# Kernel optimization log

Measured on AMD Instinct MI355X. Metric: run time of the kernel, lower is better.

Reference implementation:

```python
import jax, jax.numpy as jnp
import numpy as np

B, T, U, K, CDIM, S, M = 128, 600, 96, 10, 80, 512, 20
D1 = 3 + CDIM        # rnn1 input: x_t (3) + attention window w (CDIM)
D2 = 3 + S + CDIM    # rnn2 / rnn3 input: x_t + prev rnn out + w
OUT_DIM = 1 + 6 * M


def setup_inputs() -> dict:
    key = jax.random.key(0)
    ks = jax.random.split(key, 16)
    g = lambda k, shape: jax.random.normal(k, shape, jnp.float32) * 0.05
    z = lambda n: jnp.zeros((n,), jnp.float32)
    return {
        "x": jax.random.normal(ks[0], (B, T, 3), jnp.float32),
        "c_vec": jax.random.uniform(ks[1], (B, U, CDIM), jnp.float32),
        # FF cell 1 (input dim D1)
        "W_jx1": g(ks[2], (D1, S)), "b_jx1": z(S),
        "W_jh1": g(ks[3], (S, S)),  "b_jh1": z(S),
        "W_kx1": g(ks[4], (D1, S)), "b_kx1": z(S),
        "W_kh1": g(ks[5], (S, S)),  "b_kh1": z(S),
        # FF cell 2 (input dim D2) -- also used for the 3rd RNN (source reuses self.rnn2)
        "W_jx2": g(ks[6], (D2, S)), "b_jx2": z(S),
        "W_jh2": g(ks[7], (S, S)),  "b_jh2": z(S),
        "W_kx2": g(ks[8], (D2, S)), "b_kx2": z(S),
        "W_kh2": g(ks[9], (S, S)),  "b_kh2": z(S),
        # attention window head: S -> 3K
        "W_win": g(ks[10], (S, 3 * K)), "b_win": z(3 * K),
        # output head: S -> 1 + 6M
        "W_lin": g(ks[11], (S, OUT_DIM)), "b_lin": z(OUT_DIM),
    }


def _ff(inp, h, Wjx, bjx, Wjh, bjh, Wkx, bkx, Wkh, bkh):
    # custom gated cell: out = j*(1-h) + (1-k)*h
    j = jax.nn.sigmoid(inp @ Wjx + bjx + h @ Wjh + bjh)
    k = jax.nn.sigmoid(inp @ Wkx + bkx + h @ Wkh + bkh)
    return j * (1.0 - h) + (1.0 - k) * h


def reference(x, c_vec,
              W_jx1, b_jx1, W_jh1, b_jh1, W_kx1, b_kx1, W_kh1, b_kh1,
              W_jx2, b_jx2, W_jh2, b_jh2, W_kx2, b_kx2, W_kh2, b_kh2,
              W_win, b_win, W_lin, b_lin):
    u = jnp.arange(U, dtype=x.dtype)  # [U]

    def step(carry, xt):
        h1, h2, h3, kappa, w = carry  # h*: [B,S], kappa: [B,K], w: [B,CDIM]
        in1 = jnp.concatenate([xt, w], axis=-1)
        h1 = _ff(in1, h1, W_jx1, b_jx1, W_jh1, b_jh1, W_kx1, b_kx1, W_kh1, b_kh1)
        kg = h1 @ W_win + b_win                       # [B, 3K]
        a_hat, be_hat, k_hat = jnp.split(kg, 3, axis=1)
        alpha = jnp.exp(a_hat)                        # [B,K]
        beta = jnp.exp(be_hat)
        kappa = kappa + jnp.exp(k_hat)
        # phi[b,u] = sum_k alpha * exp(-beta * (kappa - u)^2)
        phi = jnp.sum(alpha[:, :, None] *
                      jnp.exp(-beta[:, :, None] * (kappa[:, :, None] - u) ** 2),
                      axis=1)                          # [B,U]
        w = jnp.einsum('bu,buc->bc', phi, c_vec)      # [B,CDIM]
        in2 = jnp.concatenate([xt, h1, w], axis=-1)
        h2 = _ff(in2, h2, W_jx2, b_jx2, W_jh2, b_jh2, W_kx2, b_kx2, W_kh2, b_kh2)
        in3 = jnp.concatenate([xt, h2, w], axis=-1)
        # source bug kept faithfully: third RNN reuses rnn2's weights
        h3 = _ff(in3, h3, W_jx2, b_jx2, W_jh2, b_jh2, W_kx2, b_kx2, W_kh2, b_kh2)
        return (h1, h2, h3, kappa, w), h3

    zS = jnp.zeros((B, S), x.dtype)
    init = (zS, zS, zS, jnp.zeros((B, K), x.dtype), jnp.zeros((B, CDIM), x.dtype))
    _, ys = jax.lax.scan(step, init, jnp.swapaxes(x, 0, 1))  # ys: [T,B,S]
    out_cat = jnp.swapaxes(ys, 0, 1).reshape(B * T, S)
    return out_cat @ W_lin + b_lin                    # [B*T, 1+6M]
```

## Files before the change

### kernel.cpp

```cpp
#include <hip/hip_runtime.h>
#include <hip/hip_bf16.h>

typedef __bf16 bf16;
typedef __bf16 bf16x8 __attribute__((ext_vector_type(8)));
typedef float  f32x4  __attribute__((ext_vector_type(4)));

#define AS1 __attribute__((address_space(1)))
#define AS3 __attribute__((address_space(3)))

#define NT   600
#define NB   128
#define NS   512
#define NU   96
#define NK   10
#define NC   80
#define NOUT 121

#define W1X_J 0
#define W1W_J 16384
#define W1H_J 65536
#define W1X_K 327680
#define W1W_K 344064
#define W1H_K 393216
#define W2X_J 655360
#define W2W_J 671744
#define W2A_J 720896
#define W2H_J 983040
#define W2X_K 1245184
#define W2W_K 1261568
#define W2A_K 1310720
#define W2H_K 1572864
#define WWIN  1835008
#define WLIN  1851392

#define BIAS_BYTE_OFF 3833856
#define H_BYTE_OFF    3842048
#define HBUF 65536
#define FLAG_BYTE_OFF 4659200
#define BAR_BYTE_OFF  4659264

#define HSTRIDE 520

#define AUX_SC0   1
#define AUX_SC0S1 17

__device__ __forceinline__ float ldIn(const void* q, long i, int isF32) {
  if (isF32) return ((const float*)q)[i];
  return (float)((const bf16*)q)[i];
}

struct KParams {
  const void* x;
  const void* c_vec;
  const void* b_win;
  const void* b_lin;
  const bf16* W;
  const float* bias;
  bf16* h1; bf16* h2; bf16* h3;
  void* out;
  const int* flag;
  int* bar;
};

template <int AUX>
__device__ __forceinline__ void stage_tile_async(const bf16* g, bf16* lds, int tid) {
  const int w = tid >> 6, lane = tid & 63;
#pragma unroll
  for (int r = 0; r < 4; ++r) {
    const int row = (w << 2) + r;
    __builtin_amdgcn_global_load_lds(
        (const AS1 void*)(g + (size_t)row * NS + (size_t)lane * 8),
        (AS3 void*)(lds + (size_t)row * HSTRIDE), 16, 0, AUX);
  }
}

__device__ __forceinline__ void group_arrive(int* gb) {
  __syncthreads();
  if (threadIdx.x == 0) {
    if ((__hip_atomic_fetch_add(gb, 1, __ATOMIC_RELAXED, __HIP_MEMORY_SCOPE_AGENT) & 31) == 31)
      __hip_atomic_fetch_add(gb + 8, 1, __ATOMIC_RELAXED, __HIP_MEMORY_SCOPE_AGENT);
  }
}
__device__ __forceinline__ void group_wait(int* gb, int target) {
  if (threadIdx.x == 0) {
    while (__hip_atomic_load(gb + 8, __ATOMIC_RELAXED, __HIP_MEMORY_SCOPE_AGENT) < target)
      __builtin_amdgcn_s_sleep(1);
  }
  __syncthreads();
  __atomic_signal_fence(__ATOMIC_ACQ_REL);
}

__device__ __forceinline__ void storeH(unsigned* dst, unsigned v, bool fast) {
  if (fast) *dst = v;
  else __hip_atomic_store(dst, v, __ATOMIC_RELAXED, __HIP_MEMORY_SCOPE_AGENT);
}

__global__ void sniff_kernel(const unsigned short* w, int* flag) {
  __shared__ int cnt;
  if (threadIdx.x == 0) cnt = 0;
  __syncthreads();
  int c = 0;
  for (int i = threadIdx.x; i < 8192; i += 256) {
    unsigned e = (w[2 * i] >> 7) & 0xFF;
    if (e == 0xFF || e < 96) c++;
  }
  atomicAdd(&cnt, c);
  __syncthreads();
  if (threadIdx.x == 0) *flag = (cnt > 512) ? 1 : 0;
}

__global__ void prep_kernel(const void* Wjx1, const void* Wjh1, const void* Wkx1, const void* Wkh1,
                            const void* Wjx2, const void* Wjh2, const void* Wkx2, const void* Wkh2,
                            const void* Wwin, const void* Wlin,
                            const void* bjx1, const void* bjh1, const void* bkx1, const void* bkh1,
                            const void* bjx2, const void* bjh2, const void* bkx2, const void* bkh2,
                            bf16* W, float* bias,
                            bf16* h1, bf16* h2, bf16* h3, int* bar,
                            const int* flag) {
  const int isF32 = *flag;
  const int r = blockIdx.y;
  const int e = blockIdx.x * 256 + threadIdx.x;
  if (r == 16) {
    if (e < 512) {
      bias[e]        = ldIn(bjx1, e, isF32) + ldIn(bjh1, e, isF32);
      bias[512 + e]  = ldIn(bkx1, e, isF32) + ldIn(bkh1, e, isF32);
      bias[1024 + e] = ldIn(bjx2, e, isF32) + ldIn(bjh2, e, isF32);
      bias[1536 + e] = ldIn(bkx2, e, isF32) + ldIn(bkh2, e, isF32);
    }
    return;
  }
  if (r == 17) {
    if (e < HBUF) {
      h1[e] = (bf16)0.f; h1[HBUF + e] = (bf16)0.f;
      h2[e] = (bf16)0.f; h2[HBUF + e] = (bf16)0.f;
      h3[e] = (bf16)0.f; h3[HBUF + e] = (bf16)0.f;
    }
    if (e < 1024) bar[e] = 0;
    return;
  }
  const int   row0s[16]  = {0,3,0, 0,3,0, 0,515,3,0, 0,515,3,0, 0,0};
  const int   klens[16]  = {3,80,512, 3,80,512, 3,80,512,512, 3,80,512,512, 512,512};
  const int   kpads[16]  = {32,96,512, 32,96,512, 32,96,512,512, 32,96,512,512, 512,512};
  const int   cpads[16]  = {512,512,512, 512,512,512, 512,512,512,512, 512,512,512,512, 32,128};
  const int   nsrcs[16]  = {512,512,512, 512,512,512, 512,512,512,512, 512,512,512,512, 30,121};
  const long  offs[16]   = {W1X_J,W1W_J,W1H_J, W1X_K,W1W_K,W1H_K,
                            W2X_J,W2W_J,W2A_J,W2H_J, W2X_K,W2W_K,W2A_K,W2H_K, WWIN,WLIN};
  const void* srcs[16]   = {Wjx1,Wjx1,Wjh1, Wkx1,Wkx1,Wkh1,
                            Wjx2,Wjx2,Wjx2,Wjh2, Wkx2,Wkx2,Wkx2,Wkh2, Wwin,Wlin};
  const int Kpad = kpads[r], cp = cpads[r];
  const long tot = (long)Kpad * cp;
  if (e >= tot) return;
  const int j    = e & 7;
  const int lane = (e >> 3) & 63;
  const int rest = e >> 9;
  const int kbs  = Kpad >> 5;
  const int kb   = rest % kbs;
  const int slab = rest / kbs;
  const int col  = slab * 16 + (lane & 15);
  const int k    = kb * 32 + ((lane >> 4) << 3) + j;
  const int Klen = klens[r], row0 = row0s[r], N = nsrcs[r];
  bf16 v = (bf16)0.f;
  if (k < Klen && col < N) v = (bf16)ldIn(srcs[r], (long)(row0 + k) * N + col, isF32);
  W[offs[r] + e] = v;
}

__device__ __forceinline__ void accum_term(f32x4& acc, int& cnt, int kh,
    const bf16* Arow, int astride, const bf16* B, int kbs,
    int lr, int ko, int lane) {
  for (int kb = 0; kb < kbs; ++kb) {
    if (((cnt++) & 1) != kh) continue;
    bf16x8 a = *(const bf16x8*)(Arow + (size_t)lr * astride + kb * 32 + ko);
    bf16x8 b = *(const bf16x8*)(B + ((size_t)kb * 64 + lane) * 8);
    acc = __builtin_amdgcn_mfma_f32_16x16x32_bf16(a, b, acc, 0, 0, 0);
  }
}

__device__ __forceinline__ void accStore(float* d, const f32x4& a) {
  d[0] = a[0]; d[1] = a[1]; d[2] = a[2]; d[3] = a[3];
}

__global__ __launch_bounds__(256) void scan_kernel(KParams p) {
  const int isF32 = *p.flag;
  const int tid  = threadIdx.x;
  const int wid  = tid >> 6;
  const int lane = tid & 63;
  const int wg   = blockIdx.x;
  const int m    = wg & 7;
  const int slab = wg >> 3;
  const int m16  = m << 4;
  const int lr   = lane & 15;
  const int ko   = (lane >> 4) << 3;
  const int g    = wid >> 1;
  const int kh   = wid & 1;

  unsigned* hg1w = (unsigned*)p.h1;
  unsigned* hg2w = (unsigned*)p.h2;
  unsigned* hg3w = (unsigned*)p.h3;

  __shared__ alignas(16) bf16 wLds[32768];
  __shared__ alignas(16) bf16 h1L[16 * HSTRIDE];
  __shared__ alignas(16) bf16 h2L[16 * HSTRIDE];
  __shared__ alignas(16) bf16 h3L[16 * HSTRIDE];
  __shared__ alignas(16) bf16 xtR[4][16][32];
  __shared__ alignas(16) bf16 wR[3][16][96];
  __shared__ float kapL[16][NK];
  __shared__ float alphaL[16][NK];
  __shared__ float betaL[16][NK];
  __shared__ float phiL[16][NU];
  __shared__ float accA[4][64][5];
  __shared__ float accB[4][64][5];
  __shared__ float accC[4][64][5];
  __shared__ bf16  hOut1[16][16];
  __shared__ bf16  hOut2[16][16];
  __shared__ bf16  hOut3[16][16];

  for (int i = tid; i < 4 * 16 * 32; i += 256) (&xtR[0][0][0])[i] = (bf16)0.f;
  for (int i = tid; i < 3 * 16 * 96; i += 256) (&wR[0][0][0])[i] = (bf16)0.f;
  for (int i = tid; i < 16 * NK; i += 256) (&kapL[0][0])[i] = 0.f;

  const size_t oX2 = g ? W2X_K : W2X_J, oW2 = g ? W2W_K : W2W_J;
  const size_t oX1 = g ? W1X_K : W1X_J, oW1 = g ? W1W_K : W1W_J, oH1 = g ? W1H_K : W1H_J;
  const bf16* wA2 = wLds + (g ? 8192 : 0);
  const bf16* wH2 = wLds + (g ? 24576 : 16384);

  {
    const bf16* wsrc[4] = { p.W + W2A_J + (size_t)slab * (16 * NS),
                            p.W + W2A_K + (size_t)slab * (16 * NS),
                            p.W + W2H_J + (size_t)slab * (16 * NS),
                            p.W + W2H_K + (size_t)slab * (16 * NS) };
#pragma unroll
    for (int mt = 0; mt < 4; ++mt) {
#pragma unroll
      for (int r = 0; r < 4; ++r) {
        const int chunk = (wid << 2) + r;
        __builtin_amdgcn_global_load_lds(
            (const AS1 void*)(wsrc[mt] + chunk * 512 + lane * 8),
            (AS3 void*)(wLds + mt * 8192 + chunk * 512), 16, 0, 0);
      }
    }
  }
  if (tid < 48) {
    int row = tid / 3, d = tid - row * 3;
    xtR[0][row][d] = (bf16)ldIn(p.x, ((long)(m16 + row) * NT + 0) * 3 + d, isF32);
  }
  __syncthreads();

  int* gb = p.bar + m * 64;
  {
    int xcc = __builtin_amdgcn_s_getreg((3 << 11) | (0 << 6) | 20) & 31;
    if (tid == 0) {
      __hip_atomic_fetch_or((unsigned*)(gb + 32), 1u << xcc,
                            __ATOMIC_RELAXED, __HIP_MEMORY_SCOPE_AGENT);
      __threadfence();
      if ((__hip_atomic_fetch_add(gb + 16, 1, __ATOMIC_RELAXED, __HIP_MEMORY_SCOPE_AGENT) & 31) == 31)
        __hip_atomic_fetch_add(gb + 24, 1, __ATOMIC_RELAXED, __HIP_MEMORY_SCOPE_AGENT);
      while (__hip_atomic_load(gb + 24, __ATOMIC_RELAXED, __HIP_MEMORY_SCOPE_AGENT) < 1)
        __builtin_amdgcn_s_sleep(1);
    }
    __syncthreads();
  }
  const unsigned msk = __hip_atomic_load((unsigned*)(gb + 32),
                                         __ATOMIC_RELAXED, __HIP_MEMORY_SCOPE_AGENT);
  const bool fast = (msk & (msk - 1)) == 0;

  f32x4 acc2pre = {0.f, 0.f, 0.f, 0.f};
  int bt = 0;

  {
    f32x4 acc = {0.f, 0.f, 0.f, 0.f};
    int cnt = 0;
    accum_term(acc, cnt, kh, &xtR[0][0][0], 32, p.W + oX1 + (size_t)slab * NS,       1, lr, ko, lane);
    accum_term(acc, cnt, kh, &wR[0][0][0],  96, p.W + oW1 + (size_t)slab * (3 * NS), 3, lr, ko, lane);
    accStore(accB[wid][lane], acc);
    __syncthreads();
    {
      int ls = tid & 63, r = tid >> 6;
      int s = (slab << 4) + (ls & 15);
      int rowIdx = ((ls >> 4) << 2) + r;
      float jp = accB[0][ls][r] + accB[1][ls][r] + p.bias[0 + s];
      float jj = 1.f / (1.f + __expf(-jp));
      hOut1[rowIdx][ls & 15] = (bf16)jj;
    }
    __syncthreads();
    if (tid < 128) {
      int row = tid >> 3, c = tid & 7;
      union { unsigned u; unsigned short s[2]; } v;
      union { bf16 b; unsigned short s; } a0, a1;
      a0.b = hOut1[row][2 * c]; a1.b = hOut1[row][2 * c + 1];
      v.s[0] = a0.s; v.s[1] = a1.s;
      storeH(hg1w + (m16 + row) * 256 + slab * 8 + c, v.u, fast);
    }
    ++bt;
    group_arrive(gb);
    group_wait(gb, bt);
  }

  for (int i = 0; i <= NT + 2; ++i) {
    const bool A1  = (i <= NT - 1);
    const bool AF1 = (i <= NT - 2);
    const bool A2  = (i >= 1 && i <= NT);
    const bool A3  = (i >= 2 && i <= NT + 1);
    const bool AO  = (i >= 3) && (slab < 8);
    const bool APRE = (i <= NT - 1);

    if (i >= 1 && i <= NT + 1) {
      const bf16* g2 = p.h2 + (size_t)(i & 1) * HBUF + (size_t)m16 * NS;
      if (fast) stage_tile_async<AUX_SC0>(g2, h2L, tid);
      else      stage_tile_async<AUX_SC0S1>(g2, h2L, tid);
    }
    if (i >= 2) {
      const bf16* g3 = p.h3 + (size_t)((i + 1) & 1) * HBUF + (size_t)m16 * NS;
      if (fast) stage_tile_async<AUX_SC0>(g3, h3L, tid);
      else      stage_tile_async<AUX_SC0S1>(g3, h3L, tid);
    }
    if (A1) {
      const bf16* g1 = p.h1 + (size_t)(i & 1) * HBUF + (size_t)m16 * NS;
      if (fast) stage_tile_async<AUX_SC0>(g1, h1L, tid);
      else      stage_tile_async<AUX_SC0S1>(g1, h1L, tid);
    }
    if (i <= NT - 2 && tid < 48) {
      int row = tid / 3, d = tid - row * 3;
      xtR[(i + 1) & 3][row][d] = (bf16)ldIn(p.x, ((long)(m16 + row) * NT + (i + 1)) * 3 + d, isF32);
    }
    __syncthreads();

    if (A2) {
      f32x4 acc = acc2pre;
      int cnt = 20;
      accum_term(acc, cnt, kh, h2L, HSTRIDE, wH2, 16, lr, ko, lane);
      accStore(accA[wid][lane], acc);
    }
    if (A3) {
      f32x4 acc = {0.f, 0.f, 0.f, 0.f};
      int cnt = 0;
      accum_term(acc, cnt, kh, &xtR[(i - 2) & 3][0][0], 32, p.W + oX2 + (size_t)slab * NS,      1,  lr, ko, lane);
      accum_term(acc, cnt, kh, h2L, HSTRIDE, wA2, 16, lr, ko, lane);
      accum_term(acc, cnt, kh, &wR[(i - 2) % 3][0][0], 96, p.W + oW2 + (size_t)slab * (3 * NS), 3,  lr, ko, lane);
      accum_term(acc, cnt, kh, h3L, HSTRIDE, wH2, 16, lr, ko, lane);
      accStore(accC[wid][lane], acc);
    }
    if (A1) {
      int n2 = wid & 1, kh2 = wid >> 1;
      f32x4 acc = {0.f, 0.f, 0.f, 0.f};
      const bf16* B = p.W + WWIN + (size_t)n2 * (16 * NS);
      for (int kb = 0; kb < 16; ++kb) {
        if ((kb & 1) != kh2) continue;
        bf16x8 a = *(const bf16x8*)(h1L + (size_t)lr * HSTRIDE + kb * 32 + ko);
        bf16x8 b = *(const bf16x8*)(B + ((size_t)kb * 64 + lane) * 8);
        acc = __builtin_amdgcn_mfma_f32_16x16x32_bf16(a, b, acc, 0, 0, 0);
      }
      accStore(accB[wid][lane], acc);
    }
    __syncthreads();

    const int arow = tid >> 4, aj = tid & 15;
    int ulo, uhi;
    {
      if (A2) {
        int ls = tid & 63, r = tid >> 6;
        int s = (slab << 4) + (ls & 15);
        int rowIdx = ((ls >> 4) << 2) + r;
        float jp = accA[0][ls][r] + accA[1][ls][r] + p.bias[1024 + s];
        float kp = accA[2][ls][r] + accA[3][ls][r] + p.bias[1536 + s];
        float ho = (float)h2L[rowIdx * HSTRIDE + s];
        float jj = 1.f / (1.f + __expf(-jp));
        float kk = 1.f / (1.f + __expf(-kp));
        hOut2[rowIdx][ls & 15] = (bf16)(jj * (1.f - ho) + (1.f - kk) * ho);
      }
      if (A3) {
        int ls = tid & 63, r = tid >> 6;
        int s = (slab << 4) + (ls & 15);
        int rowIdx = ((ls >> 4) << 2) + r;
        float jp = accC[0][ls][r] + accC[1][ls][r] + p.bias[1024 + s];
        float kp = accC[2][ls][r] + accC[3][ls][r] + p.bias[1536 + s];
        float ho = (float)h3L[rowIdx * HSTRIDE + s];
        float jj = 1.f / (1.f + __expf(-jp));
        float kk = 1.f / (1.f + __expf(-kp));
        hOut3[rowIdx][ls & 15] = (bf16)(jj * (1.f - ho) + (1.f - kk) * ho);
      }
      float lo = 1e30f, hi = -1e30f;
      if (A1 && aj < NK) {
        const int rr = arow & 3;
        const int lbase = (arow >> 2) << 4;
        const int o0 = aj, o1 = NK + aj, o2 = 2 * NK + aj;
        float ah    = accB[o0 >> 4][lbase | (o0 & 15)][rr] + accB[(o0 >> 4) + 2][lbase | (o0 & 15)][rr]
                    + ldIn(p.b_win, o0, isF32);
        float bepre = accB[o1 >> 4][lbase | (o1 & 15)][rr] + accB[(o1 >> 4) + 2][lbase | (o1 & 15)][rr]
                    + ldIn(p.b_win, o1, isF32);
        float dkpre = accB[o2 >> 4][lbase | (o2 & 15)][rr] + accB[(o2 >> 4) + 2][lbase | (o2 & 15)][rr]
                    + ldIn(p.b_win, o2, isF32);
        float be = expf(bepre);
        float dk = expf(dkpre);
        float al = expf(ah);
        float kap = kapL[arow][aj] + dk;
        kapL[arow][aj] = kap;
        alphaL[arow][aj] = al;
        betaL[arow][aj] = be;
        float arg = (ah + 18.42f) / be;
        if (arg > 0.f) { float R = sqrtf(arg); lo = kap - R; hi = kap + R; }
      }
      lo = fminf(lo, __shfl_xor(lo, 1));  hi = fmaxf(hi, __shfl_xor(hi, 1));
      lo = fminf(lo, __shfl_xor(lo, 2));  hi = fmaxf(hi, __shfl_xor(hi, 2));
      lo = fminf(lo, __shfl_xor(lo, 4));  hi = fmaxf(hi, __shfl_xor(hi, 4));
      lo = fminf(lo, __shfl_xor(lo, 8));  hi = fmaxf(hi, __shfl_xor(hi, 8));
      ulo = (lo <= 0.f) ? 0 : ((lo > 95.f) ? 96 : (int)floorf(lo));
      uhi = (hi >= 95.f) ? 95 : ((hi < 0.f) ? -1 : (int)ceilf(hi));
    }
    __syncthreads();

    if (A1) {
      for (int u = ulo + aj; u <= uhi; u += 16) {
        float s = 0.f, uf = (float)u;
        for (int k2 = 0; k2 < NK; ++k2) {
          float d = kapL[arow][k2] - uf;
          s += alphaL[arow][k2] * __expf(-betaL[arow][k2] * d * d);
        }
        phiL[arow][u] = s;
      }
    }
    if (A2 && tid < 128) {
      int row = tid >> 3, c = tid & 7;
      union { unsigned u; unsigned short s[2]; } v;
      union { bf16 b; unsigned short s; } a0, a1;
      a0.b = hOut2[row][2 * c]; a1.b = hOut2[row][2 * c + 1];
      v.s[0] = a0.s; v.s[1] = a1.s;
      storeH(hg2w + (size_t)((i - 1) & 1) * (HBUF / 2) + (m16 + row) * 256 + slab * 8 + c, v.u, fast);
    }
    if (A3 && tid >= 128) {
      int t2 = tid - 128;
      int row = t2 >> 3, c = t2 & 7;
      union { unsigned u; unsigned short s[2]; } v;
      union { bf16 b; unsigned short s; } a0, a1;
      a0.b = hOut3[row][2 * c]; a1.b = hOut3[row][2 * c + 1];
      v.s[0] = a0.s; v.s[1] = a1.s;
      storeH(hg3w + (size_t)((i - 2) & 1) * (HBUF / 2) + (m16 + row) * 256 + slab * 8 + c, v.u, fast);
    }
    __syncthreads();

    if (A1) {
      bf16* wOut = &wR[i % 3][0][0];
      if (isF32) {
        const float* cv = (const float*)p.c_vec + (long)(m16 + arow) * NU * NC;
        for (int ch = aj; ch < 20; ch += 16) {
          float a0 = 0.f, a1 = 0.f, a2 = 0.f, a3 = 0.f;
          for (int u = ulo; u <= uhi; ++u) {
            const float* q = cv + (long)u * NC + (ch << 2);
            float ph = phiL[arow][u];
            a0 += ph * q[0]; a1 += ph * q[1]; a2 += ph * q[2]; a3 += ph * q[3];
          }
          wOut[arow * 96 + (ch << 2) + 0] = (bf16)a0;
          wOut[arow * 96 + (ch << 2) + 1] = (bf16)a1;
          wOut[arow * 96 + (ch << 2) + 2] = (bf16)a2;
          wOut[arow * 96 + (ch << 2) + 3] = (bf16)a3;
        }
      } else {
        const long cv0 = (long)(m16 + arow) * NU * NC;
        for (int c = aj; c < NC; c += 16) {
          float acc = 0.f;
          for (int u = ulo; u <= uhi; ++u)
            acc += phiL[arow][u] * ldIn(p.c_vec, cv0 + (long)u * NC + c, isF32);
          wOut[arow * 96 + c] = (bf16)acc;
        }
      }
    }
    __syncthreads();

    if (AF1) {
      f32x4 acc = {0.f, 0.f, 0.f, 0.f};
      int cnt = 0;
      accum_term(acc, cnt, kh, &xtR[(i + 1) & 3][0][0], 32, p.W + oX1 + (size_t)slab * NS,      1,  lr, ko, lane);
      accum_term(acc, cnt, kh, &wR[i % 3][0][0], 96, p.W + oW1 + (size_t)slab * (3 * NS),       3,  lr, ko, lane);
      accum_term(acc, cnt, kh, h1L, HSTRIDE, p.W + oH1 + (size_t)slab * (16 * NS), 16, lr, ko, lane);
      accStore(accB[wid][lane], acc);
    }
    __syncthreads();

    if (AF1) {
      int ls = tid & 63, r = tid >> 6;
      int s = (slab << 4) + (ls & 15);
      int rowIdx = ((ls >> 4) << 2) + r;
      float jp = accB[0][ls][r] + accB[1][ls][r] + p.bias[0 + s];
      float kp = accB[2][ls][r] + accB[3][ls][r] + p.bias[512 + s];
      float ho = (float)h1L[rowIdx * HSTRIDE + s];
      float jj = 1.f / (1.f + __expf(-jp));
      float kk = 1.f / (1.f + __expf(-kp));
      hOut1[rowIdx][ls & 15] = (bf16)(jj * (1.f - ho) + (1.f - kk) * ho);
    }
    __syncthreads();

    if (AF1 && tid < 128) {
      int row = tid >> 3, c = tid & 7;
      union { unsigned u; unsigned short s[2]; } v;
      union { bf16 b; unsigned short s; } a0, a1;
      a0.b = hOut1[row][2 * c]; a1.b = hOut1[row][2 * c + 1];
      v.s[0] = a0.s; v.s[1] = a1.s;
      storeH(hg1w + (size_t)((i + 1) & 1) * (HBUF / 2) + (m16 + row) * 256 + slab * 8 + c, v.u, fast);
    }
    if (i < NT + 2) { ++bt; group_arrive(gb); }
    else            __syncthreads();
    if (APRE) {
      f32x4 a = {0.f, 0.f, 0.f, 0.f};
      int cnt = 0;
      accum_term(a, cnt, kh, &xtR[i & 3][0][0], 32, p.W + oX2 + (size_t)slab * NS,      1,  lr, ko, lane);
      accum_term(a, cnt, kh, h1L, HSTRIDE, wA2, 16, lr, ko, lane);
      accum_term(a, cnt, kh, &wR[i % 3][0][0], 96, p.W + oW2 + (size_t)slab * (3 * NS), 3,  lr, ko, lane);
      acc2pre = a;
    }
    if (AO) {
      f32x4 acc = {0.f, 0.f, 0.f, 0.f};
      const bf16* B = p.W + WLIN + (size_t)slab * (16 * NS);
      for (int kb = 0; kb < 16; ++kb) {
        if ((kb & 3) != wid) continue;
        bf16x8 a = *(const bf16x8*)(h3L + (size_t)lr * HSTRIDE + kb * 32 + ko);
        bf16x8 b = *(const bf16x8*)(B + ((size_t)kb * 64 + lane) * 8);
        acc = __builtin_amdgcn_mfma_f32_16x16x32_bf16(a, b, acc, 0, 0, 0);
      }
      accStore(accA[wid][lane], acc);
    }
    if (i >= 3 && slab < 8) {
      __syncthreads();
      if (tid < 64) {
        int o = (slab << 4) + (tid & 15);
        if (o < NOUT) {
          float bl = ldIn(p.b_lin, o, isF32);
          int rb = (tid >> 4) << 2;
          for (int r = 0; r < 4; ++r) {
            float v = accA[0][tid][r] + accA[1][tid][r] + accA[2][tid][r] + accA[3][tid][r] + bl;
            long oi = ((long)(m16 + rb + r) * NT + (i - 3)) * NOUT + o;
            if (isF32) ((float*)p.out)[oi] = v; else ((bf16*)p.out)[oi] = (bf16)v;
          }
        }
      }
    }
    if (i < NT + 2) group_wait(gb, bt);
  }
}

extern "C" void kernel_launch(void* const* d_in, const int* in_sizes, int n_in,
                              void* d_out, int out_size, void* d_ws, size_t ws_size,
                              hipStream_t stream) {
  (void)in_sizes; (void)n_in; (void)out_size; (void)ws_size;

  bf16*  wsW  = (bf16*)d_ws;
  float* bias = (float*)((char*)d_ws + BIAS_BYTE_OFF);
  bf16*  h1   = (bf16*)((char*)d_ws + H_BYTE_OFF);
  bf16*  h2   = h1 + 2 * HBUF;
  bf16*  h3   = h2 + 2 * HBUF;
  int*   flag = (int*)((char*)d_ws + FLAG_BYTE_OFF);
  int*   bar  = (int*)((char*)d_ws + BAR_BYTE_OFF);

  sniff_kernel<<<1, 256, 0, stream>>>((const unsigned short*)d_in[4], flag);

  prep_kernel<<<dim3(1024, 18), 256, 0, stream>>>(
      d_in[2], d_in[4], d_in[6], d_in[8], d_in[10], d_in[12], d_in[14], d_in[16],
      d_in[18], d_in[20],
      d_in[3], d_in[5], d_in[7], d_in[9], d_in[11], d_in[13], d_in[15], d_in[17],
      wsW, bias, h1, h2, h3, bar, flag);

  KParams kp;
  kp.x = d_in[0]; kp.c_vec = d_in[1]; kp.b_win = d_in[19]; kp.b_lin = d_in[21];
  kp.W = wsW; kp.bias = bias;
  kp.h1 = h1; kp.h2 = h2; kp.h3 = h3;
  kp.out = d_out;
  kp.flag = flag;
  kp.bar = bar;

  scan_kernel<<<256, 256, 0, stream>>>(kp);
}
```

Before: 9.675 ms.

## Split batch into 8-row groups across 512 workgroups, stream weights from global

Halves the batch rows per workgroup (16 to 8), doubling the grid to 512 workgroups with two per CU, and drops the 64KB LDS-resident rnn2 weight tiles so weights are read from global/L2 each step instead. MFMA tiles stay 16-wide, so half of each A-tile repeats rows and does redundant work. The goal is more parallelism and shorter per-step latency per workgroup. The cost is twice the total weight traffic through L2, wasted MFMA lanes, and a group barrier that is now 16 groups of 32. The barrier counting (&31) and the m*64 barrier indexing still assume 32 workgroups per group and may now be inconsistent with 16 groups.

Measured after the change: 15.77 ms. +63.0%, slower.

```diff
diff --git a/kernel.cpp b/kernel.cpp
--- a/kernel.cpp
+++ b/kernel.cpp
@@ -15,6 +15,7 @@
 #define NK   10
 #define NC   80
 #define NOUT 121
+#define NR   8
 
 #define W1X_J 0
 #define W1W_J 16384
@@ -66,8 +67,8 @@
 __device__ __forceinline__ void stage_tile_async(const bf16* g, bf16* lds, int tid) {
   const int w = tid >> 6, lane = tid & 63;
 #pragma unroll
-  for (int r = 0; r < 4; ++r) {
-    const int row = (w << 2) + r;
+  for (int r = 0; r < 2; ++r) {
+    const int row = (w << 1) + r;
     __builtin_amdgcn_global_load_lds(
         (const AS1 void*)(g + (size_t)row * NS + (size_t)lane * 8),
         (AS3 void*)(lds + (size_t)row * HSTRIDE), 16, 0, AUX);
@@ -179,16 +180,17 @@
   d[0] = a[0]; d[1] = a[1]; d[2] = a[2]; d[3] = a[3];
 }
 
-__global__ __launch_bounds__(256) void scan_kernel(KParams p) {
+__global__ __launch_bounds__(256, 2) void scan_kernel(KParams p) {
   const int isF32 = *p.flag;
   const int tid  = threadIdx.x;
   const int wid  = tid >> 6;
   const int lane = tid & 63;
   const int wg   = blockIdx.x;
-  const int m    = wg & 7;
-  const int slab = wg >> 3;
-  const int m16  = m << 4;
+  const int m    = wg & 15;
+  const int slab = wg >> 4;
+  const int m8   = m << 3;
   const int lr   = lane & 15;
+  const int lra  = lr & 7;
   const int ko   = (lane >> 4) << 3;
   const int g    = wid >> 1;
   const int kh   = wid & 1;
@@ -197,51 +199,34 @@
   unsigned* hg2w = (unsigned*)p.h2;
   unsigned* hg3w = (unsigned*)p.h3;
 
-  __shared__ alignas(16) bf16 wLds[32768];
-  __shared__ alignas(16) bf16 h1L[16 * HSTRIDE];
-  __shared__ alignas(16) bf16 h2L[16 * HSTRIDE];
-  __shared__ alignas(16) bf16 h3L[16 * HSTRIDE];
-  __shared__ alignas(16) bf16 xtR[4][16][32];
-  __shared__ alignas(16) bf16 wR[3][16][96];
-  __shared__ float kapL[16][NK];
-  __shared__ float alphaL[16][NK];
-  __shared__ float betaL[16][NK];
-  __shared__ float phiL[16][NU];
+  __shared__ alignas(16) bf16 h1L[NR * HSTRIDE];
+  __shared__ alignas(16) bf16 h2L[NR * HSTRIDE];
+  __shared__ alignas(16) bf16 h3L[NR * HSTRIDE];
+  __shared__ alignas(16) bf16 xtR[4][NR][32];
+  __shared__ alignas(16) bf16 wR[3][NR][96];
+  __shared__ float kapL[NR][NK];
+  __shared__ float alphaL[NR][NK];
+  __shared__ float betaL[NR][NK];
+  __shared__ float phiL[NR][NU];
   __shared__ float accA[4][64][5];
   __shared__ float accB[4][64][5];
   __shared__ float accC[4][64][5];
-  __shared__ bf16  hOut1[16][16];
-  __shared__ bf16  hOut2[16][16];
-  __shared__ bf16  hOut3[16][16];
-
-  for (int i = tid; i < 4 * 16 * 32; i += 256) (&xtR[0][0][0])[i] = (bf16)0.f;
-  for (int i = tid; i < 3 * 16 * 96; i += 256) (&wR[0][0][0])[i] = (bf16)0.f;
-  for (int i = tid; i < 16 * NK; i += 256) (&kapL[0][0])[i] = 0.f;
+  __shared__ bf16  hOut1[NR][16];
+  __shared__ bf16  hOut2[NR][16];
+  __shared__ bf16  hOut3[NR][16];
+
+  for (int i = tid; i < 4 * NR * 32; i += 256) (&xtR[0][0][0])[i] = (bf16)0.f;
+  for (int i = tid; i < 3 * NR * 96; i += 256) (&wR[0][0][0])[i] = (bf16)0.f;
+  for (int i = tid; i < NR * NK; i += 256) (&kapL[0][0])[i] = 0.f;
 
   const size_t oX2 = g ? W2X_K : W2X_J, oW2 = g ? W2W_K : W2W_J;
   const size_t oX1 = g ? W1X_K : W1X_J, oW1 = g ? W1W_K : W1W_J, oH1 = g ? W1H_K : W1H_J;
-  const bf16* wA2 = wLds + (g ? 8192 : 0);
-  const bf16* wH2 = wLds + (g ? 24576 : 16384);
-
-  {
-    const bf16* wsrc[4] = { p.W + W2A_J + (size_t)slab * (16 * NS),
-                            p.W + W2A_K + (size_t)slab * (16 * NS),
-                            p.W + W2H_J + (size_t)slab * (16 * NS),
-                            p.W + W2H_K + (size_t)slab * (16 * NS) };
-#pragma unroll
-    for (int mt = 0; mt < 4; ++mt) {
-#pragma unroll
-      for (int r = 0; r < 4; ++r) {
-        const int chunk = (wid << 2) + r;
-        __builtin_amdgcn_global_load_lds(
-            (const AS1 void*)(wsrc[mt] + chunk * 512 + lane * 8),
-            (AS3 void*)(wLds + mt * 8192 + chunk * 512), 16, 0, 0);
-      }
-    }
-  }
-  if (tid < 48) {
+  const bf16* wA2 = p.W + (g ? W2A_K : W2A_J) + (size_t)slab * (16 * NS);
+  const bf16* wH2 = p.W + (g ? W2H_K : W2H_J) + (size_t)slab * (16 * NS);
+
+  if (tid < 24) {
     int row = tid / 3, d = tid - row * 3;
-    xtR[0][row][d] = (bf16)ldIn(p.x, ((long)(m16 + row) * NT + 0) * 3 + d, isF32);
+    xtR[0][row][d] = (bf16)ldIn(p.x, ((long)(m8 + row) * NT + 0) * 3 + d, isF32);
   }
   __syncthreads();
 
@@ -269,26 +254,28 @@
   {
     f32x4 acc = {0.f, 0.f, 0.f, 0.f};
     int cnt = 0;
-    accum_term(acc, cnt, kh, &xtR[0][0][0], 32, p.W + oX1 + (size_t)slab * NS,       1, lr, ko, lane);
-    accum_term(acc, cnt, kh, &wR[0][0][0],  96, p.W + oW1 + (size_t)slab * (3 * NS), 3, lr, ko, lane);
+    accum_term(acc, cnt, kh, &xtR[0][0][0], 32, p.W + oX1 + (size_t)slab * NS,       1, lra, ko, lane);
+    accum_term(acc, cnt, kh, &wR[0][0][0],  96, p.W + oW1 + (size_t)slab * (3 * NS), 3, lra, ko, lane);
     accStore(accB[wid][lane], acc);
     __syncthreads();
     {
       int ls = tid & 63, r = tid >> 6;
-      int s = (slab << 4) + (ls & 15);
-      int rowIdx = ((ls >> 4) << 2) + r;
-      float jp = accB[0][ls][r] + accB[1][ls][r] + p.bias[0 + s];
-      float jj = 1.f / (1.f + __expf(-jp));
-      hOut1[rowIdx][ls & 15] = (bf16)jj;
-    }
-    __syncthreads();
-    if (tid < 128) {
+      if (ls < 32) {
+        int s = (slab << 4) + (ls & 15);
+        int rowIdx = ((ls >> 4) << 2) + r;
+        float jp = accB[0][ls][r] + accB[1][ls][r] + p.bias[0 + s];
+        float jj = 1.f / (1.f + __expf(-jp));
+        hOut1[rowIdx][ls & 15] = (bf16)jj;
+      }
+    }
+    __syncthreads();
+    if (tid < 64) {
       int row = tid >> 3, c = tid & 7;
       union { unsigned u; unsigned short s[2]; } v;
       union { bf16 b; unsigned short s; } a0, a1;
       a0.b = hOut1[row][2 * c]; a1.b = hOut1[row][2 * c + 1];
       v.s[0] = a0.s; v.s[1] = a1.s;
-      storeH(hg1w + (m16 + row) * 256 + slab * 8 + c, v.u, fast);
+      storeH(hg1w + (m8 + row) * 256 + slab * 8 + c, v.u, fast);
     }
     ++bt;
     group_arrive(gb);
@@ -304,39 +291,39 @@
     const bool APRE = (i <= NT - 1);
 
     if (i >= 1 && i <= NT + 1) {
-      const bf16* g2 = p.h2 + (size_t)(i & 1) * HBUF + (size_t)m16 * NS;
+      const bf16* g2 = p.h2 + (size_t)(i & 1) * HBUF + (size_t)m8 * NS;
       if (fast) stage_tile_async<AUX_SC0>(g2, h2L, tid);
       else      stage_tile_async<AUX_SC0S1>(g2, h2L, tid);
     }
     if (i >= 2) {
-      const bf16* g3 = p.h3 + (size_t)((i + 1) & 1) * HBUF + (size_t)m16 * NS;
+      const bf16* g3 = p.h3 + (size_t)((i + 1) & 1) * HBUF + (size_t)m8 * NS;
       if (fast) stage_tile_async<AUX_SC0>(g3, h3L, tid);
       else      stage_tile_async<AUX_SC0S1>(g3, h3L, tid);
     }
     if (A1) {
-      const bf16* g1 = p.h1 + (size_t)(i & 1) * HBUF + (size_t)m16 * NS;
+      const bf16* g1 = p.h1 + (size_t)(i & 1) * HBUF + (size_t)m8 * NS;
       if (fast) stage_tile_async<AUX_SC0>(g1, h1L, tid);
       else      stage_tile_async<AUX_SC0S1>(g1, h1L, tid);
     }
-    if (i <= NT - 2 && tid < 48) {
+    if (i <= NT - 2 && tid < 24) {
       int row = tid / 3, d = tid - row * 3;
-      xtR[(i + 1) & 3][row][d] = (bf16)ldIn(p.x, ((long)(m16 + row) * NT + (i + 1)) * 3 + d, isF32);
+      xtR[(i + 1) & 3][row][d] = (bf16)ldIn(p.x, ((long)(m8 + row) * NT + (i + 1)) * 3 + d, isF32);
     }
     __syncthreads();
 
     if (A2) {
       f32x4 acc = acc2pre;
       int cnt = 20;
-      accum_term(acc, cnt, kh, h2L, HSTRIDE, wH2, 16, lr, ko, lane);
+      accum_term(acc, cnt, kh, h2L, HSTRIDE, wH2, 16, lra, ko, lane);
       accStore(accA[wid][lane], acc);
     }
     if (A3) {
       f32x4 acc = {0.f, 0.f, 0.f, 0.f};
       int cnt = 0;
-      accum_term(acc, cnt, kh, &xtR[(i - 2) & 3][0][0], 32, p.W + oX2 + (size_t)slab * NS,      1,  lr, ko, lane);
-      accum_term(acc, cnt, kh, h2L, HSTRIDE, wA2, 16, lr, ko, lane);
-      accum_term(acc, cnt, kh, &wR[(i - 2) % 3][0][0], 96, p.W + oW2 + (size_t)slab * (3 * NS), 3,  lr, ko, lane);
-      accum_term(acc, cnt, kh, h3L, HSTRIDE, wH2, 16, lr, ko, lane);
+      accum_term(acc, cnt, kh, &xtR[(i - 2) & 3][0][0], 32, p.W + oX2 + (size_t)slab * NS,      1,  lra, ko, lane);
+      accum_term(acc, cnt, kh, h2L, HSTRIDE, wA2, 16, lra, ko, lane);
+      accum_term(acc, cnt, kh, &wR[(i - 2) % 3][0][0], 96, p.W + oW2 + (size_t)slab * (3 * NS), 3,  lra, ko, lane);
+      accum_term(acc, cnt, kh, h3L, HSTRIDE, wH2, 16, lra, ko, lane);
       accStore(accC[wid][lane], acc);
     }
     if (A1) {
@@ -345,7 +332,7 @@
       const bf16* B = p.W + WWIN + (size_t)n2 * (16 * NS);
       for (int kb = 0; kb < 16; ++kb) {
         if ((kb & 1) != kh2) continue;
-        bf16x8 a = *(const bf16x8*)(h1L + (size_t)lr * HSTRIDE + kb * 32 + ko);
+        bf16x8 a = *(const bf16x8*)(h1L + (size_t)lra * HSTRIDE + kb * 32 + ko);
         bf16x8 b = *(const bf16x8*)(B + ((size_t)kb * 64 + lane) * 8);
         acc = __builtin_amdgcn_mfma_f32_16x16x32_bf16(a, b, acc, 0, 0, 0);
       }
@@ -356,8 +343,8 @@
     const int arow = tid >> 4, aj = tid & 15;
     int ulo, uhi;
     {
-      if (A2) {
-        int ls = tid & 63, r = tid >> 6;
+      int ls = tid & 63, r = tid >> 6;
+      if (A2 && ls < 32) {
         int s = (slab << 4) + (ls & 15);
         int rowIdx = ((ls >> 4) << 2) + r;
         float jp = accA[0][ls][r] + accA[1][ls][r] + p.bias[1024 + s];
@@ -367,8 +354,7 @@
         float kk = 1.f / (1.f + __expf(-kp));
         hOut2[rowIdx][ls & 15] = (bf16)(jj * (1.f - ho) + (1.f - kk) * ho);
       }
-      if (A3) {
-        int ls = tid & 63, r = tid >> 6;
+      if (A3 && ls < 32) {
         int s = (slab << 4) + (ls & 15);
         int rowIdx = ((ls >> 4) << 2) + r;
         float jp = accC[0][ls][r] + accC[1][ls][r] + p.bias[1024 + s];
@@ -379,7 +365,7 @@
         hOut3[rowIdx][ls & 15] = (bf16)(jj * (1.f - ho) + (1.f - kk) * ho);
       }
       float lo = 1e30f, hi = -1e30f;
-      if (A1 && aj < NK) {
+      if (A1 && arow < NR && aj < NK) {
         const int rr = arow & 3;
         const int lbase = (arow >> 2) << 4;
         const int o0 = aj, o1 = NK + aj, o2 = 2 * NK + aj;
@@ -408,7 +394,7 @@
     }
     __syncthreads();
 
-    if (A1) {
+    if (A1 && arow < NR) {
       for (int u = ulo + aj; u <= uhi; u += 16) {
         float s = 0.f, uf = (float)u;
         for (int k2 = 0; k2 < NK; ++k2) {
@@ -418,29 +404,29 @@
         phiL[arow][u] = s;
       }
     }
-    if (A2 && tid < 128) {
+    if (A2 && tid < 64) {
       int row = tid >> 3, c = tid & 7;
       union { unsigned u; unsigned short s[2]; } v;
       union { bf16 b; unsigned short s; } a0, a1;
       a0.b = hOut2[row][2 * c]; a1.b = hOut2[row][2 * c + 1];
       v.s[0] = a0.s; v.s[1] = a1.s;
-      storeH(hg2w + (size_t)((i - 1) & 1) * (HBUF / 2) + (m16 + row) * 256 + slab * 8 + c, v.u, fast);
-    }
-    if (A3 && tid >= 128) {
+      storeH(hg2w + (size_t)((i - 1) & 1) * (HBUF / 2) + (m8 + row) * 256 + slab * 8 + c, v.u, fast);
+    }
+    if (A3 && tid >= 128 && tid < 192) {
       int t2 = tid - 128;
       int row = t2 >> 3, c = t2 & 7;
       union { unsigned u; unsigned short s[2]; } v;
       union { bf16 b; unsigned short s; } a0, a1;
       a0.b = hOut3[row][2 * c]; a1.b = hOut3[row][2 * c + 1];
       v.s[0] = a0.s; v.s[1] = a1.s;
-      storeH(hg3w + (size_t)((i - 2) & 1) * (HBUF / 2) + (m16 + row) * 256 + slab * 8 + c, v.u, fast);
-    }
-    __syncthreads();
-
-    if (A1) {
+      storeH(hg3w + (size_t)((i - 2) & 1) * (HBUF / 2) + (m8 + row) * 256 + slab * 8 + c, v.u, fast);
+    }
+    __syncthreads();
+
+    if (A1 && arow < NR) {
       bf16* wOut = &wR[i % 3][0][0];
       if (isF32) {
-        const float* cv = (const float*)p.c_vec + (long)(m16 + arow) * NU * NC;
+        const float* cv = (const float*)p.c_vec + (long)(m8 + arow) * NU * NC;
         for (int ch = aj; ch < 20; ch += 16) {
           float a0 = 0.f, a1 = 0.f, a2 = 0.f, a3 = 0.f;
           for (int u = ulo; u <= uhi; ++u) {
@@ -454,7 +440,7 @@
           wOut[arow * 96 + (ch << 2) + 3] = (bf16)a3;
         }
       } else {
-        const long cv0 = (long)(m16 + arow) * NU * NC;
+        const long cv0 = (long)(m8 + arow) * NU * NC;
         for (int c = aj; c < NC; c += 16) {
           float acc = 0.f;
           for (int u = ulo; u <= uhi; ++u)
@@ -468,42 +454,44 @@
     if (AF1) {
       f32x4 acc = {0.f, 0.f, 0.f, 0.f};
       int cnt = 0;
-      accum_term(acc, cnt, kh, &xtR[(i + 1) & 3][0][0], 32, p.W + oX1 + (size_t)slab * NS,      1,  lr, ko, lane);
-      accum_term(acc, cnt, kh, &wR[i % 3][0][0], 96, p.W + oW1 + (size_t)slab * (3 * NS),       3,  lr, ko, lane);
-      accum_term(acc, cnt, kh, h1L, HSTRIDE, p.W + oH1 + (size_t)slab * (16 * NS), 16, lr, ko, lane);
+      accum_term(acc, cnt, kh, &xtR[(i + 1) & 3][0][0], 32, p.W + oX1 + (size_t)slab * NS,      1,  lra, ko, lane);
+      accum_term(acc, cnt, kh, &wR[i % 3][0][0], 96, p.W + oW1 + (size_t)slab * (3 * NS),       3,  lra, ko, lane);
+      accum_term(acc, cnt, kh, h1L, HSTRIDE, p.W + oH1 + (size_t)slab * (16 * NS), 16, lra, ko, lane);
       accStore(accB[wid][lane], acc);
     }
     __syncthreads();
 
     if (AF1) {
       int ls = tid & 63, r = tid >> 6;
-      int s = (slab << 4) + (ls & 15);
-      int rowIdx = ((ls >> 4) << 2) + r;
-      float jp = accB[0][ls][r] + accB[1][ls][r] + p.bias[0 + s];
-      float kp = accB[2][ls][r] + accB[3][ls][r] + p.bias[512 + s];
-      float ho = (float)h1L[rowIdx * HSTRIDE + s];
-      float jj = 1.f / (1.f + __expf(-jp));
-      float kk = 1.f / (1.f + __expf(-kp));
-      hOut1[rowIdx][ls & 15] = (bf16)(jj * (1.f - ho) + (1.f - kk) * ho);
-    }
-    __syncthreads();
-
-    if (AF1 && tid < 128) {
+      if (ls < 32) {
+        int s = (slab << 4) + (ls & 15);
+        int rowIdx = ((ls >> 4) << 2) + r;
+        float jp = accB[0][ls][r] + accB[1][ls][r] + p.bias[0 + s];
+        float kp = accB[2][ls][r] + accB[3][ls][r] + p.bias[512 + s];
+        float ho = (float)h1L[rowIdx * HSTRIDE + s];
+        float jj = 1.f / (1.f + __expf(-jp));
+        float kk = 1.f / (1.f + __expf(-kp));
+        hOut1[rowIdx][ls & 15] = (bf16)(jj * (1.f - ho) + (1.f - kk) * ho);
+      }
+    }
+    __syncthreads();
+
+    if (AF1 && tid < 64) {
       int row = tid >> 3, c = tid & 7;
       union { unsigned u; unsigned short s[2]; } v;
       union { bf16 b; unsigned short s; } a0, a1;
       a0.b = hOut1[row][2 * c]; a1.b = hOut1[row][2 * c + 1];
       v.s[0] = a0.s; v.s[1] = a1.s;
-      storeH(hg1w + (size_t)((i + 1) & 1) * (HBUF / 2) + (m16 + row) * 256 + slab * 8 + c, v.u, fast);
+      storeH(hg1w + (size_t)((i + 1) & 1) * (HBUF / 2) + (m8 + row) * 256 + slab * 8 + c, v.u, fast);
     }
     if (i < NT + 2) { ++bt; group_arrive(gb); }
     else            __syncthreads();
     if (APRE) {
       f32x4 a = {0.f, 0.f, 0.f, 0.f};
       int cnt = 0;
-      accum_term(a, cnt, kh, &xtR[i & 3][0][0], 32, p.W + oX2 + (size_t)slab * NS,      1,  lr, ko, lane);
-      accum_term(a, cnt, kh, h1L, HSTRIDE, wA2, 16, lr, ko, lane);
-      accum_term(a, cnt, kh, &wR[i % 3][0][0], 96, p.W + oW2 + (size_t)slab * (3 * NS), 3,  lr, ko, lane);
+      accum_term(a, cnt, kh, &xtR[i & 3][0][0], 32, p.W + oX2 + (size_t)slab * NS,      1,  lra, ko, lane);
+      accum_term(a, cnt, kh, h1L, HSTRIDE, wA2, 16, lra, ko, lane);
+      accum_term(a, cnt, kh, &wR[i % 3][0][0], 96, p.W + oW2 + (size_t)slab * (3 * NS), 3,  lra, ko, lane);
       acc2pre = a;
     }
     if (AO) {
@@ -511,7 +499,7 @@
       const bf16* B = p.W + WLIN + (size_t)slab * (16 * NS);
       for (int kb = 0; kb < 16; ++kb) {
         if ((kb & 3) != wid) continue;
-        bf16x8 a = *(const bf16x8*)(h3L + (size_t)lr * HSTRIDE + kb * 32 + ko);
+        bf16x8 a = *(const bf16x8*)(h3L + (size_t)lra * HSTRIDE + kb * 32 + ko);
         bf16x8 b = *(const bf16x8*)(B + ((size_t)kb * 64 + lane) * 8);
         acc = __builtin_amdgcn_mfma_f32_16x16x32_bf16(a, b, acc, 0, 0, 0);
       }
@@ -519,14 +507,14 @@
     }
     if (i >= 3 && slab < 8) {
       __syncthreads();
-      if (tid < 64) {
+      if (tid < 32) {
         int o = (slab << 4) + (tid & 15);
         if (o < NOUT) {
           float bl = ldIn(p.b_lin, o, isF32);
           int rb = (tid >> 4) << 2;
           for (int r = 0; r < 4; ++r) {
             float v = accA[0][tid][r] + accA[1][tid][r] + accA[2][tid][r] + accA[3][tid][r] + bl;
-            long oi = ((long)(m16 + rb + r) * NT + (i - 3)) * NOUT + o;
+            long oi = ((long)(m8 + rb + r) * NT + (i - 3)) * NOUT + o;
             if (isF32) ((float*)p.out)[oi] = v; else ((bf16*)p.out)[oi] = (bf16)v;
           }
         }
@@ -565,5 +553,5 @@
   kp.flag = flag;
   kp.bar = bar;
 
-  scan_kernel<<<256, 256, 0, stream>>>(kp);
-}
+  scan_kernel<<<512, 256, 0, stream>>>(kp);
+}
```
